# Optimization experiments

Measured on AMD Instinct MI355X. Metric: run time of the kernel, lower is better.

The kernel has to match this reference:

```python
import jax, jax.numpy as jnp
import numpy as np

B, N, T, H, L = 4, 800, 16, 16, 1  # batch, nodes, T=in_dim/2, hidden_dim, latent_dim
TEMP = 0.2
BN_EPS = 1e-5
SLOPE = 0.01  # torch leaky_relu default


def _xavier(k, fan_out, fan_in):
    lim = float(np.sqrt(6.0 / (fan_in + fan_out)))
    return jax.random.uniform(k, (fan_out, fan_in), jnp.float32, -lim, lim)


def setup_inputs() -> dict:
    key = jax.random.key(0)
    ks = jax.random.split(key, 10)
    return {
        "x": jax.random.normal(ks[0], (B, N, T), jnp.float32),
        "u": jax.random.uniform(ks[1], (B, N, N), jnp.float32, 1e-6, 1.0 - 1e-6),
        "W_enc": _xavier(ks[2], H, T), "b_enc": jnp.zeros((H,), jnp.float32),
        "W1": _xavier(ks[3], H, 2 * H), "b1": jnp.zeros((H,), jnp.float32),
        "Wb": _xavier(ks[4], L, H), "bb": jnp.zeros((L,), jnp.float32),
        "Wmu": _xavier(ks[5], L, H), "bmu": jnp.zeros((L,), jnp.float32),
        "Wlv": _xavier(ks[6], L, H), "blv": jnp.zeros((L,), jnp.float32),
        "bn_w": jnp.ones((N,), jnp.float32), "bn_b": jnp.zeros((N,), jnp.float32),
        "W2": _xavier(ks[7], H, L), "b2": jnp.zeros((H,), jnp.float32),
        "W3": _xavier(ks[8], 2 * H, H), "b3": jnp.zeros((2 * H,), jnp.float32),
    }


def reference(x, u, W_enc, b_enc, W1, b1, Wb, bb, Wmu, bmu, Wlv, blv, bn_w, bn_b, W2, b2, W3, b3):
    lrelu = lambda v: jax.nn.leaky_relu(v, SLOPE)
    # node encoder: (B,N,T) -> (B,N,H)
    h0 = lrelu(jnp.einsum('bnt,ht->bnh', x, W_enc) + b_enc)
    # all-pairs broadcast + concat: (B,N,N,2H)
    x_pair = jnp.concatenate([
        jnp.broadcast_to(h0[:, :, None, :], (B, N, N, H)),
        jnp.broadcast_to(h0[:, None, :, :], (B, N, N, H)),
    ], axis=-1)
    # encode: fc1 + relu
    h = jax.nn.relu(jnp.einsum('bijk,hk->bijh', x_pair, W1) + b1)
    # BatchNorm2d(N): channel axis is 1 (first N); biased var, training-mode stats
    mean = h.mean(axis=(0, 2, 3), keepdims=True)
    var = h.var(axis=(0, 2, 3), keepdims=True)
    h = (h - mean) / jnp.sqrt(var + BN_EPS) * bn_w[None, :, None, None] + bn_b[None, :, None, None]
    p = jax.nn.sigmoid(jnp.einsum('bijh,lh->bijl', h, Wb) + bb)[..., 0]  # (B,N,N)
    mu = jnp.tanh(jnp.einsum('bijh,lh->bijl', h, Wmu) + bmu)        # computed, unused downstream
    logvar = jax.nn.softplus(jnp.einsum('bijh,lh->bijl', h, Wlv) + blv)  # computed, unused
    # relaxed Bernoulli sample (binary concrete), temperature 0.2
    logits = jnp.log(p) - jnp.log1p(-p)
    noise = jnp.log(u) - jnp.log1p(-u)
    z = jax.nn.sigmoid((logits + noise) / TEMP)  # (B,N,N)
    # decode
    hd = lrelu(jnp.einsum('bijl,hl->bijh', z[..., None], W2) + b2)
    recon = jnp.einsum('bijh,oh->bijo', hd, W3) + b3  # (B,N,N,2H)
    adj = z.mean(axis=0)  # (N,N)
    loss_recon = jnp.mean((recon - x_pair) ** 2)
    return (adj, loss_recon)
```

## Files before the change

kernel.cpp:

```cpp
#include <hip/hip_runtime.h>
#include <math.h>

#define B_ 4
#define N_ 800
#define H_ 16

#define WS_AP   0
#define WS_BM   51200
#define WS_P    102400
#define WS_Q    153600
#define WS_D1   204800
#define WS_D2   208000
#define WS_S    211200
#define WS_S2   212000
#define WS_SC   213072
#define WS_SS   213074
#define WS_WM   213090
#define WS_BMK  213362
#define WS_ABC  213634
#define WS_PP   213702
#define WS_QQ   322502
#define WS_ACC  431302

__global__ __launch_bounds__(256) void prep_k(
    const float* __restrict__ x, const float* __restrict__ W_enc,
    const float* __restrict__ b_enc, const float* __restrict__ W1,
    const float* __restrict__ b1, const float* __restrict__ Wb,
    const float* __restrict__ b3, const float* __restrict__ W3,
    const float* __restrict__ W2, const float* __restrict__ b2,
    float* __restrict__ ws) {
  int t = threadIdx.x;
  if (blockIdx.x == 14) {
    for (int i = t; i < 1600; i += 256) ws[WS_S + i] = 0.f;
    return;
  }
  if (blockIdx.x == 13) {
    __shared__ float sG[256], sR[16], sTB[16];
    __shared__ float sWM[272], sBMk[272];
    {
      int h = t >> 4, h2 = t & 15;
      float g = 0.f;
      #pragma unroll
      for (int o = 0; o < 32; ++o) g = fmaf(W3[o*16+h], W3[o*16+h2], g);
      sG[t] = g;
    }
    if (t < 16) {
      float r = 0.f;
      #pragma unroll
      for (int o = 0; o < 32; ++o) r = fmaf(W3[o*16+t], b3[o], r);
      sR[t] = r;
    }
    if (t == 0) {
      float bb3 = 0.f;
      for (int o = 0; o < 32; ++o) bb3 = fmaf(b3[o], b3[o], bb3);
      float wsum = 0.f;
      for (int k = 0; k < 16; ++k) wsum += Wb[k];
      ws[WS_SC + 0] = bb3;
      ws[WS_SC + 1] = wsum;
      *reinterpret_cast<double*>(ws + WS_ACC) = 0.0;

      float tb[16];
      for (int hh = 0; hh < 16; ++hh) {
        float w = W2[hh], bv = b2[hh];
        float tt = (fabsf(w) > 1e-30f) ? (-bv / w) : ((bv > 0.f) ? -0.5f : 1.5f);
        tb[hh] = fminf(fmaxf(tt, -0.5f), 1.5f);
      }
      for (int a = 1; a < 16; ++a) {
        float key = tb[a]; int c = a - 1;
        while (c >= 0 && tb[c] > key) { tb[c+1] = tb[c]; --c; }
        tb[c+1] = key;
      }
      for (int hh = 0; hh < 16; ++hh) { sTB[hh] = tb[hh]; ws[WS_SS + hh] = tb[hh]; }
    }
    __syncthreads();
    for (int idx = t; idx < 272; idx += 256) {
      int k = idx >> 4, hh = idx & 15;
      float lo = (k == 0)  ? sTB[0]  - 1.f : sTB[k-1];
      float hi = (k == 16) ? sTB[15] + 1.f : sTB[k];
      float zr = 0.5f * (lo + hi);
      float v = fmaf(zr, W2[hh], b2[hh]);
      float m = (v > 0.f) ? 1.f : 0.01f;
      float wmv = m * W2[hh], bmv = m * b2[hh];
      sWM[idx] = wmv; sBMk[idx] = bmv;
      ws[WS_WM  + idx] = wmv;
      ws[WS_BMK + idx] = bmv;
    }
    __syncthreads();
    if (t < 17) {
      int k = t;
      float A = 0.f, Bq = 0.f, Cq = 0.f, wr = 0.f, br = 0.f;
      #pragma unroll
      for (int h = 0; h < 16; ++h) {
        float wm = sWM[k*16 + h], bm = sBMk[k*16 + h];
        float gw = 0.f, gb = 0.f;
        #pragma unroll
        for (int h2 = 0; h2 < 16; ++h2) {
          float g = sG[h*16 + h2];
          gw = fmaf(g, sWM[k*16 + h2],  gw);
          gb = fmaf(g, sBMk[k*16 + h2], gb);
        }
        A  = fmaf(wm, gw, A);
        Bq = fmaf(wm, gb, Bq);
        Cq = fmaf(bm, gb, Cq);
        wr = fmaf(wm, sR[h], wr);
        br = fmaf(bm, sR[h], br);
      }
      ws[WS_ABC + k*4 + 0] = A;
      ws[WS_ABC + k*4 + 1] = 2.f * (Bq + wr);
      ws[WS_ABC + k*4 + 2] = Cq + 2.f * br;
      ws[WS_ABC + k*4 + 3] = 0.f;
    }
    return;
  }
  int row = blockIdx.x * 256 + t;
  if (row >= B_ * N_) return;
  float xr[16];
  #pragma unroll
  for (int q = 0; q < 4; ++q) {
    float4 v = *reinterpret_cast<const float4*>(x + row*16 + q*4);
    xr[q*4+0] = v.x; xr[q*4+1] = v.y; xr[q*4+2] = v.z; xr[q*4+3] = v.w;
  }
  float h0[16];
  #pragma unroll
  for (int h = 0; h < 16; ++h) {
    float a = b_enc[h];
    #pragma unroll
    for (int k = 0; k < 16; ++k) a = fmaf(xr[k], W_enc[h*16+k], a);
    h0[h] = fmaxf(a, 0.01f * a);
  }
  #pragma unroll
  for (int h = 0; h < 16; ++h) {
    float a = b1[h], bm = 0.f;
    #pragma unroll
    for (int k = 0; k < 16; ++k) {
      a  = fmaf(h0[k], W1[h*32 + k],      a);
      bm = fmaf(h0[k], W1[h*32 + 16 + k], bm);
    }
    ws[WS_AP + row*16 + h] = a;
    ws[WS_BM + row*16 + h] = bm;
  }
  #pragma unroll
  for (int h = 0; h < 16; ++h) {
    float pp = 0.f, qq = 0.f;
    #pragma unroll
    for (int o = 0; o < 16; ++o) {
      pp = fmaf(W3[o*16 + h],      h0[o], pp);
      qq = fmaf(W3[(16+o)*16 + h], h0[o], qq);
    }
    ws[WS_P + row*16 + h] = pp;
    ws[WS_Q + row*16 + h] = qq;
  }
  float c1 = 0.f, c2 = 0.f, e = 0.f;
  #pragma unroll
  for (int o = 0; o < 16; ++o) {
    c1 = fmaf(b3[o],    h0[o], c1);
    c2 = fmaf(b3[16+o], h0[o], c2);
    e  = fmaf(h0[o],    h0[o], e);
  }
  ws[WS_D1 + row] = e - 2.f * c1;
  ws[WS_D2 + row] = e - 2.f * c2;
}

__global__ __launch_bounds__(256) void stats_proj_k(float* __restrict__ ws) {
  int t = threadIdx.x;
  int blk = blockIdx.x;
  if (blk >= 200) {
    int idx = (blk - 200) * 256 + t;
    if (idx >= 3200 * 17) return;
    int row = idx / 17, k = idx - row * 17;
    const float* wm = ws + WS_WM  + k*16;
    const float* bm = ws + WS_BMK + k*16;
    const float* Pr = ws + WS_P + row*16;
    const float* Qr = ws + WS_Q + row*16;
    float pw = 0.f, pb = 0.f, qw = 0.f, qb = 0.f;
    #pragma unroll
    for (int h = 0; h < 16; ++h) {
      float p = Pr[h], q = Qr[h], w = wm[h], b = bm[h];
      pw = fmaf(w, p, pw); pb = fmaf(b, p, pb);
      qw = fmaf(w, q, qw); qb = fmaf(b, q, qb);
    }
    ws[WS_PP + idx*2 + 0] = pw;
    ws[WS_PP + idx*2 + 1] = pb;
    ws[WS_QQ + idx*2 + 0] = qw;
    ws[WS_QQ + idx*2 + 1] = qb;
    return;
  }
  int it = blk >> 2, js = blk & 3;
  int i0 = it * 16, jbase = js * 200;
  __shared__ __align__(16) float sBMs[4][200][20];
  __shared__ __align__(16) float sAt[4][16][16];
  for (int idx = t; idx < 3200; idx += 256) {
    int r = idx >> 2, q = idx & 3;
    int b = r / 200, l = r - b*200;
    *reinterpret_cast<float4*>(&sBMs[b][l][q*4]) =
        *reinterpret_cast<const float4*>(ws + WS_BM + (b*N_ + jbase + l)*16 + q*4);
  }
  {
    int b = t >> 6, r = t & 63;
    reinterpret_cast<float4*>(&sAt[0][0][0])[t] =
        *reinterpret_cast<const float4*>(ws + WS_AP + (b*N_ + i0)*16 + r*4);
  }
  __syncthreads();
  int il = t >> 4, jt = t & 15;
  float a[4][16];
  #pragma unroll
  for (int b = 0; b < 4; ++b)
    #pragma unroll
    for (int h = 0; h < 16; ++h) a[b][h] = sAt[b][il][h];
  float s = 0.f, s2 = 0.f;
  for (int jj = 0; jj < 13; ++jj) {
    int j = jt + jj*16;
    if (j >= 200) break;
    #pragma unroll
    for (int b = 0; b < 4; ++b) {
      #pragma unroll
      for (int q = 0; q < 4; ++q) {
        float4 bm = *reinterpret_cast<const float4*>(&sBMs[b][j][q*4]);
        float v;
        v = fmaxf(a[b][q*4+0] + bm.x, 0.f); s += v; s2 = fmaf(v, v, s2);
        v = fmaxf(a[b][q*4+1] + bm.y, 0.f); s += v; s2 = fmaf(v, v, s2);
        v = fmaxf(a[b][q*4+2] + bm.z, 0.f); s += v; s2 = fmaf(v, v, s2);
        v = fmaxf(a[b][q*4+3] + bm.w, 0.f); s += v; s2 = fmaf(v, v, s2);
      }
    }
  }
  #pragma unroll
  for (int off = 8; off; off >>= 1) {
    s  += __shfl_down(s,  off, 16);
    s2 += __shfl_down(s2, off, 16);
  }
  if (jt == 0) {
    atomicAdd(ws + WS_S  + i0 + il, s);
    atomicAdd(ws + WS_S2 + i0 + il, s2);
  }
}

__global__ __launch_bounds__(256) void pair_k(
    const float* __restrict__ u, const float* __restrict__ Wb,
    const float* __restrict__ bn_w, const float* __restrict__ bn_b,
    const float* __restrict__ bb, const float* __restrict__ ws,
    float* __restrict__ out, double* __restrict__ acc) {
  __shared__ __align__(16) float sAp[4][32][16];
  __shared__ __align__(16) float sBm[4][32][17];
  __shared__ __align__(16) float4 sABC[17];
  __shared__ float sd1[4][32], sd2[4][32];
  __shared__ float sAl[32], sBe[32];
  __shared__ float red[4];
  __shared__ float sbb3;

  int t  = threadIdx.x;
  int bi = blockIdx.x % 25, bj = blockIdx.x / 25;
  int i0 = bi * 32, j0 = bj * 32;
  int li = t >> 4, lj = t & 15;

  float ur[16];
  #pragma unroll
  for (int b = 0; b < 4; ++b)
    #pragma unroll
    for (int di = 0; di < 2; ++di)
      #pragma unroll
      for (int dj = 0; dj < 2; ++dj)
        ur[b*4 + di*2 + dj] = u[(b*N_ + i0 + li + di*16)*N_ + j0 + lj + dj*16];

  {
    float4* dAp = reinterpret_cast<float4*>(&sAp[0][0][0]);
    for (int idx = t; idx < 512; idx += 256) {
      int b = idx >> 7, r = idx & 127;
      dAp[idx] = *reinterpret_cast<const float4*>(ws + WS_AP + (b*N_ + i0)*16 + r*4);
    }
    for (int idx = t; idx < 2048; idx += 256) {
      int b = idx >> 9, r = idx & 511;
      int l = r >> 4, h = r & 15;
      sBm[b][l][h] = ws[WS_BM + (b*N_ + j0 + l)*16 + h];
    }
  }
  if (t < 68) reinterpret_cast<float*>(sABC)[t] = ws[WS_ABC + t];
  if (t < 128) {
    sd1[t >> 5][t & 31] = ws[WS_D1 + (t >> 5)*N_ + i0 + (t & 31)];
    sd2[t >> 5][t & 31] = ws[WS_D2 + (t >> 5)*N_ + j0 + (t & 31)];
  }
  if (t < 32) {
    float s = ws[WS_S + i0 + t], s2 = ws[WS_S2 + i0 + t];
    const float inv = 1.0f / 51200.0f;
    float mean = s * inv;
    float var  = s2 * inv - mean * mean;
    float rstd = 1.0f / sqrtf(var + 1e-5f);
    float al = bn_w[i0 + t] * rstd;
    float wsum = ws[WS_SC + 1];
    sAl[t] = al;
    sBe[t] = fmaf(-al * mean, wsum, fmaf(bn_b[i0 + t], wsum, bb[0]));
  }
  if (t == 0) sbb3 = ws[WS_SC + 0];
  float ssr[16], wbr[16];
  #pragma unroll
  for (int h = 0; h < 16; ++h) ssr[h] = ws[WS_SS + h];
  #pragma unroll
  for (int h = 0; h < 16; ++h) wbr[h] = Wb[h];
  __syncthreads();

  float al0 = sAl[li], be0 = sBe[li], al1 = sAl[li+16], be1 = sBe[li+16];
  const float* ppb0 = ws + WS_PP + (0*N_ + i0 + li)*34;
  const float* qqb0 = ws + WS_QQ + (0*N_ + j0 + lj)*34;
  float zsum[4] = {0.f, 0.f, 0.f, 0.f};
  float Lacc = 0.f;

  #pragma unroll
  for (int b = 0; b < 4; ++b) {
    float Af[2][16], Mf[2][16];
    #pragma unroll
    for (int d = 0; d < 2; ++d) {
      #pragma unroll
      for (int q = 0; q < 4; ++q) {
        float4 va = *reinterpret_cast<const float4*>(&sAp[b][li + d*16][q*4]);
        Af[d][q*4+0] = va.x; Af[d][q*4+1] = va.y; Af[d][q*4+2] = va.z; Af[d][q*4+3] = va.w;
      }
      #pragma unroll
      for (int h = 0; h < 16; ++h)
        Mf[d][h] = sBm[b][lj + d*16][h];
    }
    #pragma unroll
    for (int di = 0; di < 2; ++di) {
      #pragma unroll
      for (int dj = 0; dj < 2; ++dj) {
        float S = 0.f;
        #pragma unroll
        for (int h = 0; h < 16; ++h) {
          float v = fmaxf(Af[di][h] + Mf[dj][h], 0.f);
          S = fmaf(v, wbr[h], S);
        }
        float xl = fmaf(di ? al1 : al0, S, di ? be1 : be0);
        float uu = ur[b*4 + di*2 + dj];
        float noise = __logf(uu) - __logf(1.0f - uu);
        float z = __fdividef(1.0f, 1.0f + __expf((xl + noise) * -5.0f));
        zsum[di*2 + dj] += z;
        int kx2 = 0;
        #pragma unroll
        for (int h = 0; h < 16; ++h) kx2 += (z > ssr[h]) ? 2 : 0;
        float4 abc = sABC[kx2 >> 1];
        float2 pp = *reinterpret_cast<const float2*>(
            ppb0 + (b*N_ + di*16)*34 + kx2);
        float2 qq = *reinterpret_cast<const float2*>(
            qqb0 + (b*N_ + dj*16)*34 + kx2);
        Lacc += fmaf(abc.x, z*z, fmaf(abc.y, z, abc.z))
              - 2.f * fmaf(z, pp.x + qq.x, pp.y + qq.y);
      }
    }
  }
  #pragma unroll
  for (int b = 0; b < 4; ++b)
    Lacc += 2.f * (sd1[b][li] + sd1[b][li+16] + sd2[b][lj] + sd2[b][lj+16]);
  Lacc += 16.f * sbb3;

  #pragma unroll
  for (int di = 0; di < 2; ++di)
    #pragma unroll
    for (int dj = 0; dj < 2; ++dj)
      out[(i0 + li + di*16)*N_ + j0 + lj + dj*16] = zsum[di*2 + dj] * 0.25f;

  #pragma unroll
  for (int off = 32; off; off >>= 1) Lacc += __shfl_down(Lacc, off);
  if ((t & 63) == 0) red[t >> 6] = Lacc;
  __syncthreads();
  if (t == 0) atomicAdd(acc, (double)(red[0] + red[1] + red[2] + red[3]));
}

__global__ void fin_k(const double* __restrict__ acc, float* __restrict__ out) {
  out[N_ * N_] = (float)(*acc * (1.0 / (4.0 * 800.0 * 800.0 * 32.0)));
}

extern "C" void kernel_launch(void* const* d_in, const int* in_sizes, int n_in,
                              void* d_out, int out_size, void* d_ws, size_t ws_size,
                              hipStream_t stream) {
  const float* x     = (const float*)d_in[0];
  const float* u     = (const float*)d_in[1];
  const float* W_enc = (const float*)d_in[2];
  const float* b_enc = (const float*)d_in[3];
  const float* W1    = (const float*)d_in[4];
  const float* b1    = (const float*)d_in[5];
  const float* Wb    = (const float*)d_in[6];
  const float* bb    = (const float*)d_in[7];
  const float* bn_w  = (const float*)d_in[12];
  const float* bn_b  = (const float*)d_in[13];
  const float* W2    = (const float*)d_in[14];
  const float* b2    = (const float*)d_in[15];
  const float* W3    = (const float*)d_in[16];
  const float* b3    = (const float*)d_in[17];

  float*  out = (float*)d_out;
  float*  ws  = (float*)d_ws;
  double* acc = (double*)(ws + WS_ACC);

  prep_k      <<<15,  256, 0, stream>>>(x, W_enc, b_enc, W1, b1, Wb, b3, W3, W2, b2, ws);
  stats_proj_k<<<413, 256, 0, stream>>>(ws);
  pair_k      <<<625, 256, 0, stream>>>(u, Wb, bn_w, bn_b, bb, ws, out, acc);
  fin_k       <<<1,   1,   0, stream>>>(acc, out);
}
```

Measured before the change: 146.7 us.

## Fold final reduction into pair kernel and split stats kernel into more blocks

Drops the separate single-thread finalize kernel. The last pair_k block, found through an atomic ticket counter that prep_k zeroes, now writes the loss, which saves one kernel launch. The stats kernel is also split into 400 blocks of 100 j-columns each and reads BM straight from global memory instead of staging 64KB in shared memory, aiming for higher occupancy and more parallelism. The cost is uncached global loads in the inner loop and a threadfence/atomic handshake.

```diff
diff --git a/kernel.cpp b/kernel.cpp
--- a/kernel.cpp
+++ b/kernel.cpp
@@ -21,6 +21,7 @@
 #define WS_PP   213702
 #define WS_QQ   322502
 #define WS_ACC  431302
+#define WS_TK   431304
 
 __global__ __launch_bounds__(256) void prep_k(
     const float* __restrict__ x, const float* __restrict__ W_enc,
@@ -32,6 +33,7 @@
   int t = threadIdx.x;
   if (blockIdx.x == 14) {
     for (int i = t; i < 1600; i += 256) ws[WS_S + i] = 0.f;
+    if (t == 0) *reinterpret_cast<unsigned*>(ws + WS_TK) = 0u;
     return;
   }
   if (blockIdx.x == 13) {
@@ -164,8 +166,8 @@
 __global__ __launch_bounds__(256) void stats_proj_k(float* __restrict__ ws) {
   int t = threadIdx.x;
   int blk = blockIdx.x;
-  if (blk >= 200) {
-    int idx = (blk - 200) * 256 + t;
+  if (blk >= 400) {
+    int idx = (blk - 400) * 256 + t;
     if (idx >= 3200 * 17) return;
     int row = idx / 17, k = idx - row * 17;
     const float* wm = ws + WS_WM  + k*16;
@@ -185,16 +187,9 @@
     ws[WS_QQ + idx*2 + 1] = qb;
     return;
   }
-  int it = blk >> 2, js = blk & 3;
-  int i0 = it * 16, jbase = js * 200;
-  __shared__ __align__(16) float sBMs[4][200][20];
   __shared__ __align__(16) float sAt[4][16][16];
-  for (int idx = t; idx < 3200; idx += 256) {
-    int r = idx >> 2, q = idx & 3;
-    int b = r / 200, l = r - b*200;
-    *reinterpret_cast<float4*>(&sBMs[b][l][q*4]) =
-        *reinterpret_cast<const float4*>(ws + WS_BM + (b*N_ + jbase + l)*16 + q*4);
-  }
+  int it = blk >> 3, js = blk & 7;
+  int i0 = it * 16, jbase = js * 100;
   {
     int b = t >> 6, r = t & 63;
     reinterpret_cast<float4*>(&sAt[0][0][0])[t] =
@@ -208,19 +203,22 @@
     #pragma unroll
     for (int h = 0; h < 16; ++h) a[b][h] = sAt[b][il][h];
   float s = 0.f, s2 = 0.f;
-  for (int jj = 0; jj < 13; ++jj) {
+  #pragma unroll
+  for (int jj = 0; jj < 7; ++jj) {
     int j = jt + jj*16;
-    if (j >= 200) break;
-    #pragma unroll
-    for (int b = 0; b < 4; ++b) {
-      #pragma unroll
-      for (int q = 0; q < 4; ++q) {
-        float4 bm = *reinterpret_cast<const float4*>(&sBMs[b][j][q*4]);
-        float v;
-        v = fmaxf(a[b][q*4+0] + bm.x, 0.f); s += v; s2 = fmaf(v, v, s2);
-        v = fmaxf(a[b][q*4+1] + bm.y, 0.f); s += v; s2 = fmaf(v, v, s2);
-        v = fmaxf(a[b][q*4+2] + bm.z, 0.f); s += v; s2 = fmaf(v, v, s2);
-        v = fmaxf(a[b][q*4+3] + bm.w, 0.f); s += v; s2 = fmaf(v, v, s2);
+    if (j < 100) {
+      #pragma unroll
+      for (int b = 0; b < 4; ++b) {
+        #pragma unroll
+        for (int q = 0; q < 4; ++q) {
+          float4 bm = *reinterpret_cast<const float4*>(
+              ws + WS_BM + (b*N_ + jbase + j)*16 + q*4);
+          float v;
+          v = fmaxf(a[b][q*4+0] + bm.x, 0.f); s += v; s2 = fmaf(v, v, s2);
+          v = fmaxf(a[b][q*4+1] + bm.y, 0.f); s += v; s2 = fmaf(v, v, s2);
+          v = fmaxf(a[b][q*4+2] + bm.z, 0.f); s += v; s2 = fmaf(v, v, s2);
+          v = fmaxf(a[b][q*4+3] + bm.w, 0.f); s += v; s2 = fmaf(v, v, s2);
+        }
       }
     }
   }
@@ -238,7 +236,7 @@
 __global__ __launch_bounds__(256) void pair_k(
     const float* __restrict__ u, const float* __restrict__ Wb,
     const float* __restrict__ bn_w, const float* __restrict__ bn_b,
-    const float* __restrict__ bb, const float* __restrict__ ws,
+    const float* __restrict__ bb, float* __restrict__ ws,
     float* __restrict__ out, double* __restrict__ acc) {
   __shared__ __align__(16) float sAp[4][32][16];
   __shared__ __align__(16) float sBm[4][32][17];
@@ -299,8 +297,8 @@
   __syncthreads();
 
   float al0 = sAl[li], be0 = sBe[li], al1 = sAl[li+16], be1 = sBe[li+16];
-  const float* ppb0 = ws + WS_PP + (0*N_ + i0 + li)*34;
-  const float* qqb0 = ws + WS_QQ + (0*N_ + j0 + lj)*34;
+  const float* ppb0 = ws + WS_PP + (i0 + li)*34;
+  const float* qqb0 = ws + WS_QQ + (j0 + lj)*34;
   float zsum[4] = {0.f, 0.f, 0.f, 0.f};
   float Lacc = 0.f;
 
@@ -337,10 +335,8 @@
         #pragma unroll
         for (int h = 0; h < 16; ++h) kx2 += (z > ssr[h]) ? 2 : 0;
         float4 abc = sABC[kx2 >> 1];
-        float2 pp = *reinterpret_cast<const float2*>(
-            ppb0 + (b*N_ + di*16)*34 + kx2);
-        float2 qq = *reinterpret_cast<const float2*>(
-            qqb0 + (b*N_ + dj*16)*34 + kx2);
+        float2 pp = *reinterpret_cast<const float2*>(ppb0 + (b*N_ + di*16)*34 + kx2);
+        float2 qq = *reinterpret_cast<const float2*>(qqb0 + (b*N_ + dj*16)*34 + kx2);
         Lacc += fmaf(abc.x, z*z, fmaf(abc.y, z, abc.z))
               - 2.f * fmaf(z, pp.x + qq.x, pp.y + qq.y);
       }
@@ -361,11 +357,15 @@
   for (int off = 32; off; off >>= 1) Lacc += __shfl_down(Lacc, off);
   if ((t & 63) == 0) red[t >> 6] = Lacc;
   __syncthreads();
-  if (t == 0) atomicAdd(acc, (double)(red[0] + red[1] + red[2] + red[3]));
-}
-
-__global__ void fin_k(const double* __restrict__ acc, float* __restrict__ out) {
-  out[N_ * N_] = (float)(*acc * (1.0 / (4.0 * 800.0 * 800.0 * 32.0)));
+  if (t == 0) {
+    atomicAdd(acc, (double)(red[0] + red[1] + red[2] + red[3]));
+    __threadfence();
+    unsigned old = atomicAdd(reinterpret_cast<unsigned*>(ws + WS_TK), 1u);
+    if (old == 624u) {
+      double v = atomicAdd(acc, 0.0);
+      out[N_ * N_] = (float)(v * (1.0 / (4.0 * 800.0 * 800.0 * 32.0)));
+    }
+  }
 }
 
 extern "C" void kernel_launch(void* const* d_in, const int* in_sizes, int n_in,
@@ -391,7 +391,6 @@
   double* acc = (double*)(ws + WS_ACC);
 
   prep_k      <<<15,  256, 0, stream>>>(x, W_enc, b_enc, W1, b1, Wb, b3, W3, W2, b2, ws);
-  stats_proj_k<<<413, 256, 0, stream>>>(ws);
+  stats_proj_k<<<613, 256, 0, stream>>>(ws);
   pair_k      <<<625, 256, 0, stream>>>(u, Wb, bn_w, bn_b, bb, ws, out, acc);
-  fin_k       <<<1,   1,   0, stream>>>(acc, out);
 }
```

After: 154.8 us. 5.5% more time.
